# Performance work log

Measured on AMD Instinct MI355X. Metric: run time of the kernel, lower is better.

Reference implementation:

```python
import jax, jax.numpy as jnp
import numpy as np


def setup_inputs() -> dict:
    key = jax.random.key(0)
    k1, k2, k3, k4, k5 = jax.random.split(key, 5)
    B, S, H, V = 16, 256, 1024, 32000
    std = 0.02
    return {
        "input_ids": jax.random.randint(k1, (B, S), 0, V, dtype=jnp.int64),
        "emb": jax.random.normal(k2, (V, H), dtype=jnp.float32) * std,
        "w_hx": jax.random.normal(k3, (H, H), dtype=jnp.float32) * std,
        "w_hh": jax.random.normal(k4, (H, H), dtype=jnp.float32) * std,
        "w_yh": jax.random.normal(k5, (V, H), dtype=jnp.float32) * std,
    }


def reference(input_ids, emb, w_hx, w_hh, w_yh):
    # input_ids: [B, S] int; emb: [V, H]; w_*: torch Linear weights [out, in]
    B, S = input_ids.shape
    H = emb.shape[1]
    x = emb[input_ids]                         # [B, S, H]
    # Precompute input contribution for all timesteps: x_t @ w_hx.T
    xin = jnp.einsum('bsh,oh->bso', x, w_hx)   # [B, S, H]
    h0 = jnp.zeros((B, H), dtype=x.dtype)

    def step(h, xin_t):
        h_new = jnp.tanh(xin_t + h @ w_hh.T)   # [B, H]
        return h_new, h_new

    _, hs = jax.lax.scan(step, h0, jnp.swapaxes(xin, 0, 1))  # hs: [S, B, H]
    hs = jnp.swapaxes(hs, 0, 1)                # [B, S, H]
    logits = jnp.einsum('bsh,vh->bsv', hs, w_yh)  # [B, S, V]
    return logits
```

## Files before the change

### kernel.cpp

```cpp
#include <hip/hip_runtime.h>
#include <stdint.h>

typedef __attribute__((ext_vector_type(8)))  short   short8;
typedef __attribute__((ext_vector_type(8)))  unsigned short ushort8;
typedef __attribute__((ext_vector_type(8)))  __bf16  bf16x8;
typedef __attribute__((ext_vector_type(4)))  float   floatx4;
typedef __attribute__((ext_vector_type(4)))  unsigned short ushort4v;

#define AS1 __attribute__((address_space(1)))
#define AS3 __attribute__((address_space(3)))

__device__ __forceinline__ unsigned short f2bf(float f) {
  unsigned u = __builtin_bit_cast(unsigned, f);
  u = (u + 0x7FFFu + ((u >> 16) & 1u)) >> 16;
  return (unsigned short)u;
}
__device__ __forceinline__ float bf2f(unsigned short h) {
  unsigned u = ((unsigned)h) << 16;
  return __builtin_bit_cast(float, u);
}

__global__ __launch_bounds__(256) void convert_bf16(const float* __restrict__ src,
                                                    unsigned short* __restrict__ dst,
                                                    int n) {
  int i = (blockIdx.x * 256 + threadIdx.x) * 4;
  if (i >= n) return;
  float4 v = *(const float4*)(src + i);
  ushort4v o;
  o.x = f2bf(v.x); o.y = f2bf(v.y); o.z = f2bf(v.z); o.w = f2bf(v.w);
  *(ushort4v*)(dst + i) = o;
}

__global__ __launch_bounds__(256) void detect_i64(const int* __restrict__ idbuf,
                                                  int* __restrict__ flag) {
  int v = 0;
  for (int i = threadIdx.x; i < 2048; i += 256) v |= idbuf[2 * i + 1];
  if (v != 0) atomicOr(flag, 1);
}

__global__ __launch_bounds__(256) void gather_embed(const int* __restrict__ ids,
                                                    const float* __restrict__ emb,
                                                    unsigned short* __restrict__ xbf,
                                                    const int* __restrict__ flag) {
  int i = blockIdx.x;
  int row = (*flag != 0) ? ids[i] : ids[2 * i];
  const float* src = emb + (size_t)row * 1024 + threadIdx.x * 4;
  float4 v = *(const float4*)src;
  ushort4v o;
  o.x = f2bf(v.x); o.y = f2bf(v.y); o.z = f2bf(v.z); o.w = f2bf(v.w);
  *(ushort4v*)(xbf + (size_t)i * 1024 + threadIdx.x * 4) = o;
}

__global__ __launch_bounds__(256) void gemm_bt(const unsigned short* __restrict__ A,
                                               const unsigned short* __restrict__ B,
                                               float* __restrict__ C,
                                               int M, int N, int K) {
  __shared__ unsigned short lA[128 * 64];
  __shared__ unsigned short lB[128 * 64];
  const int nwg  = gridDim.x;
  const int wgid = blockIdx.x;
  const int q    = nwg >> 3;
  const int swz  = (wgid & 7) * q + (wgid >> 3);
  const int ntx  = N >> 7;
  const int bx   = swz % ntx;
  const int by   = swz / ntx;
  const int tid  = threadIdx.x;
  const int lane = tid & 63;
  const int w    = tid >> 6;
  const int wr   = w >> 1, wc = w & 1;

  floatx4 acc[4][4];
#pragma unroll
  for (int m = 0; m < 4; ++m)
#pragma unroll
    for (int n = 0; n < 4; ++n) acc[m][n] = (floatx4){0.f, 0.f, 0.f, 0.f};

  const size_t rowA0 = (size_t)by * 128;
  const size_t colB0 = (size_t)bx * 128;

  for (int k0 = 0; k0 < K; k0 += 64) {
#pragma unroll
    for (int p = 0; p < 4; ++p) {
      int cc = p * 256 + tid;
      int r  = cc >> 3;
      int c8 = cc & 7;
      const unsigned short* srcA = A + (rowA0 + r) * K + k0 + c8 * 8;
      const unsigned short* srcB = B + (colB0 + r) * K + k0 + c8 * 8;
      __builtin_amdgcn_global_load_lds((const AS1 unsigned int*)srcA,
                                       (AS3 unsigned int*)&lA[cc * 8], 16, 0, 0);
      __builtin_amdgcn_global_load_lds((const AS1 unsigned int*)srcB,
                                       (AS3 unsigned int*)&lB[cc * 8], 16, 0, 0);
    }
    __syncthreads();
#pragma unroll
    for (int kk = 0; kk < 2; ++kk) {
      const int kofs = kk * 32 + (lane >> 4) * 8;
      bf16x8 af[4], bfv[4];
#pragma unroll
      for (int m = 0; m < 4; ++m) {
        int r = wr * 64 + m * 16 + (lane & 15);
        af[m] = *(const bf16x8*)&lA[r * 64 + kofs];
      }
#pragma unroll
      for (int n = 0; n < 4; ++n) {
        int r = wc * 64 + n * 16 + (lane & 15);
        bfv[n] = *(const bf16x8*)&lB[r * 64 + kofs];
      }
#pragma unroll
      for (int m = 0; m < 4; ++m)
#pragma unroll
        for (int n = 0; n < 4; ++n)
          acc[m][n] = __builtin_amdgcn_mfma_f32_16x16x32_bf16(af[m], bfv[n], acc[m][n], 0, 0, 0);
    }
    __syncthreads();
  }

#pragma unroll
  for (int m = 0; m < 4; ++m) {
#pragma unroll
    for (int j = 0; j < 4; ++j) {
      size_t row = rowA0 + wr * 64 + m * 16 + ((lane >> 4) * 4 + j);
      float* crow = C + row * (size_t)N + colB0 + wc * 64 + (lane & 15);
#pragma unroll
      for (int n = 0; n < 4; ++n) crow[n * 16] = acc[m][n][j];
    }
  }
}

__global__ __launch_bounds__(1024) void rnn_step_all(const float* __restrict__ xin,
                                                     const unsigned short* __restrict__ whh_bf,
                                                     float* __restrict__ hs,
                                                     unsigned short* __restrict__ hs_bf,
                                                     unsigned int* __restrict__ flags) {
  const int b     = blockIdx.x >> 4;
  const int slice = blockIdx.x & 15;
  const int tid   = threadIdx.x;
  const int o     = tid & 63;
  const int kc    = tid >> 6;

  __shared__ __align__(16) float hl[1024];
  __shared__ float red[1024];

  float wf[64];
  {
    const unsigned short* wrow = whh_bf + (size_t)(slice * 64 + o) * 1024 + kc * 64;
#pragma unroll
    for (int j = 0; j < 8; ++j) {
      ushort8 wv = *(const ushort8*)(wrow + j * 8);
#pragma unroll
      for (int e = 0; e < 8; ++e) wf[j * 8 + e] = bf2f(wv[e]);
    }
  }

  const size_t bbase = (size_t)b * 256 * 1024;
  unsigned int* bflags = flags + b * 64;

  for (int t = 0; t < 256; ++t) {
    if (t == 0) {
      hl[tid] = 0.0f;
    } else {
      while (__hip_atomic_load(&bflags[kc], __ATOMIC_RELAXED,
                               __HIP_MEMORY_SCOPE_AGENT) < (unsigned)t) { }
      asm volatile("" ::: "memory");
      hl[tid] = __hip_atomic_load(&hs[bbase + (size_t)(t - 1) * 1024 + tid],
                                  __ATOMIC_RELAXED, __HIP_MEMORY_SCOPE_AGENT);
    }
    float sum = 0.0f;
#pragma unroll
    for (int j4 = 0; j4 < 16; ++j4) {
      float4 hv = *(const float4*)&hl[kc * 64 + j4 * 4];
      sum += wf[j4 * 4 + 0] * hv.x + wf[j4 * 4 + 1] * hv.y +
             wf[j4 * 4 + 2] * hv.z + wf[j4 * 4 + 3] * hv.w;
    }
    red[tid] = sum;
    float s = 0.0f;
    if (tid < 64) s = xin[bbase + (size_t)t * 1024 + slice * 64 + tid];
    __syncthreads();

    if (tid < 64) {
#pragma unroll
      for (int k2 = 0; k2 < 16; ++k2) s += red[k2 * 64 + tid];
      float hv   = tanhf(s);
      size_t idx = bbase + (size_t)t * 1024 + slice * 64 + tid;
      __hip_atomic_store(&hs[idx], hv, __ATOMIC_RELAXED, __HIP_MEMORY_SCOPE_AGENT);
      hs_bf[idx] = f2bf(hv);
      asm volatile("s_waitcnt vmcnt(0)" ::: "memory");
      if (tid == 0)
        __hip_atomic_store(&bflags[slice], (unsigned)(t + 1),
                           __ATOMIC_RELAXED, __HIP_MEMORY_SCOPE_AGENT);
    }
    __syncthreads();
  }
}

extern "C" void kernel_launch(void* const* d_in, const int* in_sizes, int n_in,
                              void* d_out, int out_size, void* d_ws, size_t ws_size,
                              hipStream_t stream) {
  const int*   ids  = (const int*)d_in[0];
  const float* emb  = (const float*)d_in[1];
  const float* w_hx = (const float*)d_in[2];
  const float* w_hh = (const float*)d_in[3];
  const float* w_yh = (const float*)d_in[4];
  float*       out  = (float*)d_out;

  const int B = 16, S = 256, H = 1024, V = 32000;
  const int BS = B * S;

  char*  ws  = (char*)d_ws;
  size_t off = 0;
  auto alloc = [&](size_t bytes) {
    size_t cur = off;
    off += (bytes + 255) & ~(size_t)255;
    return (void*)(ws + cur);
  };

  unsigned short* whx_bf = (unsigned short*)alloc((size_t)H * H * 2);
  unsigned short* whh_bf = (unsigned short*)alloc((size_t)H * H * 2);
  unsigned short* wyh_bf = (unsigned short*)alloc((size_t)V * H * 2);
  unsigned short* x_bf   = (unsigned short*)alloc((size_t)BS * H * 2);
  float*          xin    = (float*)alloc((size_t)BS * H * 4);
  float*          hs     = (float*)alloc((size_t)BS * H * 4);
  unsigned short* hs_bf  = (unsigned short*)alloc((size_t)BS * H * 2);
  unsigned int*   flags  = (unsigned int*)alloc(4096 + 256);
  int*            dflag  = (int*)(flags + 1024);

  hipMemsetAsync(flags, 0, 4096 + 256, stream);

  detect_i64<<<dim3(1), dim3(256), 0, stream>>>(ids, dflag);
  convert_bf16<<<dim3((H * H) / 1024), dim3(256), 0, stream>>>(w_hx, whx_bf, H * H);
  convert_bf16<<<dim3((H * H) / 1024), dim3(256), 0, stream>>>(w_hh, whh_bf, H * H);
  convert_bf16<<<dim3((V * H) / 1024), dim3(256), 0, stream>>>(w_yh, wyh_bf, V * H);
  gather_embed<<<dim3(BS), dim3(256), 0, stream>>>(ids, emb, x_bf, dflag);

  gemm_bt<<<dim3((BS / 128) * (H / 128)), dim3(256), 0, stream>>>(x_bf, whx_bf, xin, BS, H, H);

  rnn_step_all<<<dim3(256), dim3(1024), 0, stream>>>(xin, whh_bf, hs, hs_bf, flags);

  gemm_bt<<<dim3((BS / 128) * (V / 128)), dim3(256), 0, stream>>>(hs_bf, wyh_bf, out, BS, V, H);
}
```

Before: 1.070 ms.

## Replace per-slice flag polling with NaN-sentinel data polling in RNN recurrence

The separate per-slice flag array is removed. The hidden-state buffer is pre-filled with NaN (memset 0xFF), and each thread spins directly on the hs value it needs until it is no longer NaN. This cuts out the flag store, the vmcnt wait and one of the two block barriers per step, and double-buffers the reduction array so the trailing barrier is no longer needed. tanh is replaced with a fast exp/rcp formula. The extra memset of the 16 MB hs buffer adds bandwidth cost, and the sentinel scheme depends on relaxed-order visibility of the data stores.

```diff
diff --git a/kernel.cpp b/kernel.cpp
--- a/kernel.cpp
+++ b/kernel.cpp
@@ -127,11 +127,10 @@
   }
 }
 
-__global__ __launch_bounds__(1024) void rnn_step_all(const float* __restrict__ xin,
-                                                     const unsigned short* __restrict__ whh_bf,
-                                                     float* __restrict__ hs,
-                                                     unsigned short* __restrict__ hs_bf,
-                                                     unsigned int* __restrict__ flags) {
+__global__ __launch_bounds__(1024, 4) void rnn_step_all(const float* __restrict__ xin,
+                                                        const unsigned short* __restrict__ whh_bf,
+                                                        float* __restrict__ hs,
+                                                        unsigned short* __restrict__ hs_bf) {
   const int b     = blockIdx.x >> 4;
   const int slice = blockIdx.x & 15;
   const int tid   = threadIdx.x;
@@ -139,7 +138,7 @@
   const int kc    = tid >> 6;
 
   __shared__ __align__(16) float hl[1024];
-  __shared__ float red[1024];
+  __shared__ float red[2][1024];
 
   float wf[64];
   {
@@ -150,21 +149,27 @@
 #pragma unroll
       for (int e = 0; e < 8; ++e) wf[j * 8 + e] = bf2f(wv[e]);
     }
+#pragma unroll
+    for (int j = 0; j < 64; ++j) asm volatile("" : "+v"(wf[j]));
   }
 
   const size_t bbase = (size_t)b * 256 * 1024;
-  unsigned int* bflags = flags + b * 64;
 
   for (int t = 0; t < 256; ++t) {
+    float s = 0.0f;
+    if (tid < 64) s = xin[bbase + (size_t)t * 1024 + slice * 64 + tid];
+
     if (t == 0) {
       hl[tid] = 0.0f;
     } else {
-      while (__hip_atomic_load(&bflags[kc], __ATOMIC_RELAXED,
-                               __HIP_MEMORY_SCOPE_AGENT) < (unsigned)t) { }
-      asm volatile("" ::: "memory");
-      hl[tid] = __hip_atomic_load(&hs[bbase + (size_t)(t - 1) * 1024 + tid],
-                                  __ATOMIC_RELAXED, __HIP_MEMORY_SCOPE_AGENT);
-    }
+      const float* src = &hs[bbase + (size_t)(t - 1) * 1024 + (size_t)kc * 64 + o];
+      float v;
+      do {
+        v = __hip_atomic_load(src, __ATOMIC_RELAXED, __HIP_MEMORY_SCOPE_AGENT);
+      } while (__any(v != v));
+      hl[tid] = v;
+    }
+
     float sum = 0.0f;
 #pragma unroll
     for (int j4 = 0; j4 < 16; ++j4) {
@@ -172,24 +177,18 @@
       sum += wf[j4 * 4 + 0] * hv.x + wf[j4 * 4 + 1] * hv.y +
              wf[j4 * 4 + 2] * hv.z + wf[j4 * 4 + 3] * hv.w;
     }
-    red[tid] = sum;
-    float s = 0.0f;
-    if (tid < 64) s = xin[bbase + (size_t)t * 1024 + slice * 64 + tid];
+    red[t & 1][tid] = sum;
     __syncthreads();
 
     if (tid < 64) {
 #pragma unroll
-      for (int k2 = 0; k2 < 16; ++k2) s += red[k2 * 64 + tid];
-      float hv   = tanhf(s);
-      size_t idx = bbase + (size_t)t * 1024 + slice * 64 + tid;
+      for (int k2 = 0; k2 < 16; ++k2) s += red[t & 1][k2 * 64 + tid];
+      float e  = __expf(2.0f * s);
+      float hv = 1.0f - 2.0f * __builtin_amdgcn_rcpf(e + 1.0f);
+      size_t idx = bbase + (size_t)t * 1024 + (size_t)slice * 64 + tid;
       __hip_atomic_store(&hs[idx], hv, __ATOMIC_RELAXED, __HIP_MEMORY_SCOPE_AGENT);
       hs_bf[idx] = f2bf(hv);
-      asm volatile("s_waitcnt vmcnt(0)" ::: "memory");
-      if (tid == 0)
-        __hip_atomic_store(&bflags[slice], (unsigned)(t + 1),
-                           __ATOMIC_RELAXED, __HIP_MEMORY_SCOPE_AGENT);
-    }
-    __syncthreads();
+    }
   }
 }
 
@@ -221,10 +220,10 @@
   float*          xin    = (float*)alloc((size_t)BS * H * 4);
   float*          hs     = (float*)alloc((size_t)BS * H * 4);
   unsigned short* hs_bf  = (unsigned short*)alloc((size_t)BS * H * 2);
-  unsigned int*   flags  = (unsigned int*)alloc(4096 + 256);
-  int*            dflag  = (int*)(flags + 1024);
-
-  hipMemsetAsync(flags, 0, 4096 + 256, stream);
+  int*            dflag  = (int*)alloc(256);
+
+  hipMemsetAsync(hs, 0xFF, (size_t)BS * H * 4, stream);
+  hipMemsetAsync(dflag, 0, 256, stream);
 
   detect_i64<<<dim3(1), dim3(256), 0, stream>>>(ids, dflag);
   convert_bf16<<<dim3((H * H) / 1024), dim3(256), 0, stream>>>(w_hx, whx_bf, H * H);
@@ -234,7 +233,7 @@
 
   gemm_bt<<<dim3((BS / 128) * (H / 128)), dim3(256), 0, stream>>>(x_bf, whx_bf, xin, BS, H, H);
 
-  rnn_step_all<<<dim3(256), dim3(1024), 0, stream>>>(xin, whh_bf, hs, hs_bf, flags);
+  rnn_step_all<<<dim3(256), dim3(1024), 0, stream>>>(xin, whh_bf, hs, hs_bf);
 
   gemm_bt<<<dim3((BS / 128) * (V / 128)), dim3(256), 0, stream>>>(hs_bf, wyh_bf, out, BS, V, H);
 }
```

Result: faster. 931.9 us (-12.9%).
